# Performance work log

Measured on AMD Instinct MI355X. Metric: run time of the kernel, lower is better.

The kernel has to match this reference:

```python
import jax, jax.numpy as jnp
import numpy as np

N_NODES = 100000
N_EDGES = 600000
NODE_DIM = 128
EDGE_DIM = 16
OUT_DIM = 128


def setup_inputs() -> dict:
    key = jax.random.key(0)
    k1, k2, k3, k4 = jax.random.split(key, 4)
    x = jax.random.normal(k1, (N_NODES, NODE_DIM), dtype=jnp.float32)
    edge_index = jax.random.randint(k2, (2, N_EDGES), 0, N_NODES, dtype=jnp.int64)
    edge_attr = jax.random.normal(k3, (N_EDGES, EDGE_DIM), dtype=jnp.float32)
    in_dim = 2 * NODE_DIM + EDGE_DIM
    # Linear layer params (Kaiming-uniform-like scale)
    lim = 1.0 / np.sqrt(in_dim)
    W = jax.random.uniform(k4, (in_dim, OUT_DIM), minval=-lim, maxval=lim, dtype=jnp.float32)
    b = jnp.zeros((OUT_DIM,), dtype=jnp.float32)
    return {"x": x, "edge_index": edge_index, "edge_attr": edge_attr, "W": W, "b": b}


def reference(x, edge_index, edge_attr, W, b):
    # h_ij = Linear([h_i, h_j, x_ij])
    h_i = x[edge_index[0]]            # [E, node_dim]
    h_j = x[edge_index[1]]            # [E, node_dim]
    # Split the GEMM over the concat blocks to avoid materializing [E, 2D+F]
    W_i, W_j, W_e = W[:NODE_DIM], W[NODE_DIM:2 * NODE_DIM], W[2 * NODE_DIM:]
    out = h_i @ W_i + h_j @ W_j + edge_attr @ W_e + b
    return out  # [E, out_dim]
```

## Files before the change

kernel.cpp:

```cpp
#include <hip/hip_runtime.h>
#include <cstdint>
#include <cstddef>

#define NE 600000
#define NN 100000

typedef __attribute__((ext_vector_type(8)))  __bf16         bf16x8;
typedef __attribute__((ext_vector_type(16))) float          f32x16;
typedef __attribute__((ext_vector_type(8)))  unsigned short u16x8;

__device__ inline unsigned short f2bf(float f) {
    unsigned int u = __builtin_bit_cast(unsigned int, f);
    u += 0x7fffu + ((u >> 16) & 1u);
    return (unsigned short)(u >> 16);
}

__global__ void pack_w(const float* __restrict__ W, unsigned short* __restrict__ Wp) {
    int t = blockIdx.x * 256 + threadIdx.x;
    if (t >= 272 * 128) return;
    int k = t >> 7, col = t & 127;
    Wp[((k >> 3) * 128 + col) * 8 + (k & 7)] = f2bf(W[t]);
}

__global__ void cvt_x(const float* __restrict__ x, unsigned short* __restrict__ xb) {
    size_t t = (size_t)(blockIdx.x * 256 + threadIdx.x) * 8;
    float4 a = *(const float4*)(x + t);
    float4 b = *(const float4*)(x + t + 4);
    u16x8 o;
    o[0] = f2bf(a.x); o[1] = f2bf(a.y); o[2] = f2bf(a.z); o[3] = f2bf(a.w);
    o[4] = f2bf(b.x); o[5] = f2bf(b.y); o[6] = f2bf(b.z); o[7] = f2bf(b.w);
    *(u16x8*)(xb + t) = o;
}

#define WAIT_VM(n) do { asm volatile("" ::: "memory");                      \
                        __builtin_amdgcn_s_waitcnt(0x0F70 | (n));           \
                        asm volatile("" ::: "memory"); } while (0)

__global__ __launch_bounds__(256, 2) void edge_mm2(
    const unsigned short* __restrict__ xb,
    const unsigned short* __restrict__ Wp,
    const int* __restrict__ ei,
    const float* __restrict__ ea,
    const float* __restrict__ bias,
    float* __restrict__ out)
{
    __shared__ __attribute__((aligned(16))) unsigned short Abuf[4][2][32][128];

    const int lane = threadIdx.x & 63;
    const int wave = threadIdx.x >> 6;
    const int r  = lane & 31;
    const int h  = lane >> 5;
    const int g4 = lane >> 4;
    const int sl = lane & 15;
    const int ebase = blockIdx.x * 128 + wave * 32;
    if (ebase >= NE) return;
    const int e = ebase + r;

#pragma unroll
    for (int i = 0; i < 8; ++i) {
        int row = 4 * i + g4;
        int nidx = ei[ebase + row];
        const unsigned short* gs = xb + (size_t)nidx * 128 + ((sl ^ (row & 15)) << 3);
        __builtin_amdgcn_global_load_lds(
            (const __attribute__((address_space(1))) void*)gs,
            (__attribute__((address_space(3))) void*)&Abuf[wave][0][4 * i][0],
            16, 0, 0);
    }
#pragma unroll
    for (int i = 0; i < 8; ++i) {
        int row = 4 * i + g4;
        int nidx = ei[NE + ebase + row];
        const unsigned short* gs = xb + (size_t)nidx * 128 + ((sl ^ (row & 15)) << 3);
        __builtin_amdgcn_global_load_lds(
            (const __attribute__((address_space(1))) void*)gs,
            (__attribute__((address_space(3))) void*)&Abuf[wave][1][4 * i][0],
            16, 0, 0);
    }

    const float4* ae = (const float4*)(ea + (size_t)e * 16);
    float4 p = ae[2 * h], q = ae[2 * h + 1];

    f32x16 acc[4];
#pragma unroll
    for (int t = 0; t < 4; ++t)
#pragma unroll
        for (int i = 0; i < 16; ++i) acc[t][i] = 0.f;

    const bf16x8* Wg = (const bf16x8*)Wp;
    const int rm = r & 15;

    WAIT_VM(8);
#pragma unroll
    for (int S = 0; S < 8; ++S) {
        int kb = 2 * S + h;
        bf16x8 a = *(const bf16x8*)&Abuf[wave][0][r][(kb ^ rm) << 3];
#pragma unroll
        for (int t = 0; t < 4; ++t) {
            bf16x8 b = Wg[kb * 128 + t * 32 + r];
            acc[t] = __builtin_amdgcn_mfma_f32_32x32x16_bf16(a, b, acc[t], 0, 0, 0);
        }
    }

    WAIT_VM(0);
#pragma unroll
    for (int S = 0; S < 8; ++S) {
        int kb = 2 * S + h;
        bf16x8 a = *(const bf16x8*)&Abuf[wave][1][r][(kb ^ rm) << 3];
#pragma unroll
        for (int t = 0; t < 4; ++t) {
            bf16x8 b = Wg[(16 + kb) * 128 + t * 32 + r];
            acc[t] = __builtin_amdgcn_mfma_f32_32x32x16_bf16(a, b, acc[t], 0, 0, 0);
        }
    }

    {
        u16x8 o;
        o[0] = f2bf(p.x); o[1] = f2bf(p.y); o[2] = f2bf(p.z); o[3] = f2bf(p.w);
        o[4] = f2bf(q.x); o[5] = f2bf(q.y); o[6] = f2bf(q.z); o[7] = f2bf(q.w);
        bf16x8 a = __builtin_bit_cast(bf16x8, o);
#pragma unroll
        for (int t = 0; t < 4; ++t) {
            bf16x8 b = Wg[(32 + h) * 128 + t * 32 + r];
            acc[t] = __builtin_amdgcn_mfma_f32_32x32x16_bf16(a, b, acc[t], 0, 0, 0);
        }
    }

    float* orow = out + (size_t)ebase * 128;
#pragma unroll
    for (int t = 0; t < 4; ++t) {
        float bv = bias[t * 32 + r];
#pragma unroll
        for (int i = 0; i < 16; ++i) {
            int row = (i & 3) + 8 * (i >> 2) + 4 * h;
            orow[(size_t)row * 128 + t * 32 + r] = acc[t][i] + bv;
        }
    }
}

__global__ __launch_bounds__(256, 2) void edge_mm_fb(
    const float* __restrict__ x,
    const unsigned short* __restrict__ Wp,
    const int* __restrict__ ei,
    const float* __restrict__ ea,
    const float* __restrict__ bias,
    float* __restrict__ out)
{
    __shared__ unsigned short Wl[32 * 128 * 8];
    {
        const uint4* Wg = (const uint4*)Wp;
        uint4* Ws = (uint4*)Wl;
#pragma unroll
        for (int i = 0; i < 16; ++i)
            Ws[threadIdx.x + 256 * i] = Wg[threadIdx.x + 256 * i];
    }
    const int lane = threadIdx.x & 63;
    const int wave = threadIdx.x >> 6;
    const int r = lane & 31;
    const int h = lane >> 5;
    const long ebase = (long)blockIdx.x * 128 + wave * 32;
    __syncthreads();
    if (ebase >= NE) return;
    const int e = (int)ebase + r;
    const int src = ei[e];
    const int dst = ei[NE + e];
    f32x16 acc[4];
#pragma unroll
    for (int t = 0; t < 4; ++t)
#pragma unroll
        for (int i = 0; i < 16; ++i) acc[t][i] = 0.f;
    const bf16x8* Wv = (const bf16x8*)Wl;
#pragma unroll
    for (int ph = 0; ph < 2; ++ph) {
        int node = ph ? dst : src;
#pragma unroll
        for (int s = 0; s < 8; ++s) {
            const float4* ax = (const float4*)(x + (size_t)node * 128);
            float4 pp = ax[(2 * s + h) * 2], qq = ax[(2 * s + h) * 2 + 1];
            u16x8 o;
            o[0] = f2bf(pp.x); o[1] = f2bf(pp.y); o[2] = f2bf(pp.z); o[3] = f2bf(pp.w);
            o[4] = f2bf(qq.x); o[5] = f2bf(qq.y); o[6] = f2bf(qq.z); o[7] = f2bf(qq.w);
            bf16x8 a = __builtin_bit_cast(bf16x8, o);
            int S = ph * 8 + s;
#pragma unroll
            for (int t = 0; t < 4; ++t) {
                bf16x8 b = Wv[(2 * S + h) * 128 + t * 32 + r];
                acc[t] = __builtin_amdgcn_mfma_f32_32x32x16_bf16(a, b, acc[t], 0, 0, 0);
            }
        }
    }
    {
        const float4* ae = (const float4*)(ea + (size_t)e * 16);
        float4 pp = ae[2 * h], qq = ae[2 * h + 1];
        u16x8 o;
        o[0] = f2bf(pp.x); o[1] = f2bf(pp.y); o[2] = f2bf(pp.z); o[3] = f2bf(pp.w);
        o[4] = f2bf(qq.x); o[5] = f2bf(qq.y); o[6] = f2bf(qq.z); o[7] = f2bf(qq.w);
        bf16x8 a = __builtin_bit_cast(bf16x8, o);
        const bf16x8* Wg = (const bf16x8*)Wp;
#pragma unroll
        for (int t = 0; t < 4; ++t) {
            bf16x8 b = Wg[(32 + h) * 128 + t * 32 + r];
            acc[t] = __builtin_amdgcn_mfma_f32_32x32x16_bf16(a, b, acc[t], 0, 0, 0);
        }
    }
    float* orow = out + (size_t)ebase * 128;
#pragma unroll
    for (int t = 0; t < 4; ++t) {
        float bv = bias[t * 32 + r];
#pragma unroll
        for (int i = 0; i < 16; ++i) {
            int row = (i & 3) + 8 * (i >> 2) + 4 * h;
            orow[(size_t)row * 128 + t * 32 + r] = acc[t][i] + bv;
        }
    }
}

extern "C" void kernel_launch(void* const* d_in, const int* in_sizes, int n_in,
                              void* d_out, int out_size, void* d_ws, size_t ws_size,
                              hipStream_t stream) {
    const float* x  = (const float*)d_in[0];
    const int*   ei = (const int*)d_in[1];
    const float* ea = (const float*)d_in[2];
    const float* W  = (const float*)d_in[3];
    const float* b  = (const float*)d_in[4];
    float* out = (float*)d_out;

    unsigned short* Wp = (unsigned short*)d_ws;
    unsigned short* xb = (unsigned short*)((char*)d_ws + 69632);
    const size_t need = 69632 + (size_t)NN * 128 * 2;

    hipLaunchKernelGGL(pack_w, dim3(136), dim3(256), 0, stream, W, Wp);

    if (ws_size >= need) {
        hipLaunchKernelGGL(cvt_x, dim3(6250), dim3(256), 0, stream, x, xb);
        hipLaunchKernelGGL(edge_mm2, dim3(4688), dim3(256), 0, stream,
                           xb, Wp, ei, ea, b, out);
    } else {
        hipLaunchKernelGGL(edge_mm_fb, dim3(4688), dim3(256), 0, stream,
                           x, Wp, ei, ea, b, out);
    }
}
```

Before: 442.6 us.

## Precompute per-node projections, then gather-and-add per edge

Reorders the computation: a node_mm kernel first computes x@W_i and x@W_j for all 100k nodes in bf16 MFMA and stores them as fp32 Y and Z buffers. An edge_combine kernel then gathers Y[src] and Z[dst] rows per edge, adds the small 16-wide edge-attribute projection done with scalar FMAs, and writes the output. This removes the per-edge 256-deep GEMM (6x redundant over nodes) in exchange for writing and re-reading 102 MB of fp32 intermediates. It also needs a much larger workspace, and the old path is kept as a fallback.

```diff
diff --git a/kernel.cpp b/kernel.cpp
--- a/kernel.cpp
+++ b/kernel.cpp
@@ -8,6 +8,7 @@
 typedef __attribute__((ext_vector_type(8)))  __bf16         bf16x8;
 typedef __attribute__((ext_vector_type(16))) float          f32x16;
 typedef __attribute__((ext_vector_type(8)))  unsigned short u16x8;
+typedef __attribute__((ext_vector_type(2)))  float          f32x2;
 
 __device__ inline unsigned short f2bf(float f) {
     unsigned int u = __builtin_bit_cast(unsigned int, f);
@@ -31,6 +32,106 @@
     o[4] = f2bf(b.x); o[5] = f2bf(b.y); o[6] = f2bf(b.z); o[7] = f2bf(b.w);
     *(u16x8*)(xb + t) = o;
 }
+
+
+__global__ __launch_bounds__(256, 2) void node_mm(
+    const unsigned short* __restrict__ xb,
+    const unsigned short* __restrict__ Wp,
+    float* __restrict__ Y,
+    float* __restrict__ Z)
+{
+    const int lane = threadIdx.x & 63;
+    const int wave = threadIdx.x >> 6;
+    const int r = lane & 31;
+    const int h = lane >> 5;
+    const int nb = (blockIdx.x * 4 + wave) * 32;
+    if (nb >= NN) return;
+
+    const bf16x8* Wg = (const bf16x8*)Wp;
+    f32x16 accY[4], accZ[4];
+#pragma unroll
+    for (int t = 0; t < 4; ++t)
+#pragma unroll
+        for (int i = 0; i < 16; ++i) { accY[t][i] = 0.f; accZ[t][i] = 0.f; }
+
+#pragma unroll
+    for (int S = 0; S < 8; ++S) {
+        const int kb = 2 * S + h;
+        bf16x8 a = *(const bf16x8*)(xb + (size_t)(nb + r) * 128 + kb * 8);
+#pragma unroll
+        for (int t = 0; t < 4; ++t) {
+            accY[t] = __builtin_amdgcn_mfma_f32_32x32x16_bf16(
+                          a, Wg[kb * 128 + t * 32 + r],        accY[t], 0, 0, 0);
+            accZ[t] = __builtin_amdgcn_mfma_f32_32x32x16_bf16(
+                          a, Wg[(16 + kb) * 128 + t * 32 + r], accZ[t], 0, 0, 0);
+        }
+    }
+
+#pragma unroll
+    for (int t = 0; t < 4; ++t)
+#pragma unroll
+        for (int i = 0; i < 16; ++i) {
+            int row = (i & 3) + 8 * (i >> 2) + 4 * h;
+            Y[(size_t)(nb + row) * 128 + t * 32 + r] = accY[t][i];
+            Z[(size_t)(nb + row) * 128 + t * 32 + r] = accZ[t][i];
+        }
+}
+
+__global__ __launch_bounds__(256, 5) void edge_combine(
+    const float* __restrict__ Y,
+    const float* __restrict__ Z,
+    const int*   __restrict__ ei,
+    const float* __restrict__ ea,
+    const float* __restrict__ W,
+    const float* __restrict__ bias,
+    float* __restrict__ out)
+{
+    const int lane = threadIdx.x & 63;
+    const int w = (blockIdx.x * 256 + threadIdx.x) >> 6;
+    if (w >= NE / 64) return;
+    const int ebase = w * 64;
+
+    float wex[16], wey[16];
+#pragma unroll
+    for (int k = 0; k < 16; ++k) {
+        f32x2 t = *(const f32x2*)(W + (size_t)(256 + k) * 128 + 2 * lane);
+        wex[k] = t.x; wey[k] = t.y;
+    }
+    const f32x2 bv = *(const f32x2*)(bias + 2 * lane);
+
+    const int srcv = ei[ebase + lane];
+    const int dstv = ei[NE + ebase + lane];
+    const float* eab = ea + (size_t)ebase * 16;
+
+#pragma unroll 2
+    for (int jo = 0; jo < 16; ++jo) {
+        float eag = __builtin_nontemporal_load(eab + jo * 64 + lane);
+#pragma unroll
+        for (int ji = 0; ji < 4; ++ji) {
+            const int j = jo * 4 + ji;
+            const int s = __builtin_amdgcn_readlane(srcv, j);
+            const int d = __builtin_amdgcn_readlane(dstv, j);
+            f32x2 y = *(const f32x2*)(Y + ((size_t)s << 7) + 2 * lane);
+            f32x2 z = *(const f32x2*)(Z + ((size_t)d << 7) + 2 * lane);
+
+            float ax = bv.x, ay = bv.y;
+#pragma unroll
+            for (int k = 0; k < 16; ++k) {
+                int eb = __builtin_amdgcn_readlane(
+                             __builtin_bit_cast(int, eag), ji * 16 + k);
+                float e = __builtin_bit_cast(float, eb);
+                ax = fmaf(e, wex[k], ax);
+                ay = fmaf(e, wey[k], ay);
+            }
+            f32x2 o;
+            o.x = ax + y.x + z.x;
+            o.y = ay + y.y + z.y;
+            __builtin_nontemporal_store(
+                o, (f32x2*)(out + ((size_t)(ebase + j) << 7) + 2 * lane));
+        }
+    }
+}
+
 
 #define WAIT_VM(n) do { asm volatile("" ::: "memory");                      \
                         __builtin_amdgcn_s_waitcnt(0x0F70 | (n));           \
@@ -226,11 +327,20 @@
 
     unsigned short* Wp = (unsigned short*)d_ws;
     unsigned short* xb = (unsigned short*)((char*)d_ws + 69632);
-    const size_t need = 69632 + (size_t)NN * 128 * 2;
+    float* Yb = (float*)((char*)d_ws + 69632 + 25600000);
+    float* Zb = (float*)((char*)d_ws + 69632 + 25600000 + 51200000);
+
+    const size_t need_mid  = 69632 + (size_t)NN * 128 * 2;
+    const size_t need_full = need_mid + 2ull * NN * 128 * 4;
 
     hipLaunchKernelGGL(pack_w, dim3(136), dim3(256), 0, stream, W, Wp);
 
-    if (ws_size >= need) {
+    if (ws_size >= need_full) {
+        hipLaunchKernelGGL(cvt_x, dim3(6250), dim3(256), 0, stream, x, xb);
+        hipLaunchKernelGGL(node_mm, dim3(782), dim3(256), 0, stream, xb, Wp, Yb, Zb);
+        hipLaunchKernelGGL(edge_combine, dim3(2344), dim3(256), 0, stream,
+                           Yb, Zb, ei, ea, W, b, out);
+    } else if (ws_size >= need_mid) {
         hipLaunchKernelGGL(cvt_x, dim3(6250), dim3(256), 0, stream, x, xb);
         hipLaunchKernelGGL(edge_mm2, dim3(4688), dim3(256), 0, stream,
                            xb, Wp, ei, ea, b, out);
```

After: 525.0 us. +18.6%, slower.
